# Kernel tuning notes

Measured on AMD Instinct MI355X. Metric: run time of the kernel, lower is better.

## Reference

```python
import jax, jax.numpy as jnp
import numpy as np

N, K = 8192, 32
DIM_INP_Q, DIM_INP_KV, DIM, DIM_OUT = 256, 256, 256, 512


def setup_inputs() -> dict:
    key = jax.random.key(0)
    ks = jax.random.split(key, 16)
    s = lambda k_, shp: jax.random.normal(k_, shp, dtype=jnp.float32) * 0.05
    return {
        "xyz_q": jax.random.normal(ks[0], (N, 3), dtype=jnp.float32),
        "feats_q": jax.random.normal(ks[1], (N, DIM_INP_Q), dtype=jnp.float32),
        "xyz_kv": jax.random.normal(ks[2], (N, K, 3), dtype=jnp.float32),
        "feats_kv": jax.random.normal(ks[3], (N, K, DIM_INP_KV), dtype=jnp.float32),
        # linear weights stored (in, out); y = x @ W + b
        "Wq": s(ks[4], (DIM_INP_Q, DIM)),
        "Wk": s(ks[5], (DIM_INP_KV, DIM)),
        "Wv": s(ks[6], (DIM_INP_KV, DIM)),
        "d1_w": s(ks[7], (3, DIM // 2)), "d1_b": jnp.zeros((DIM // 2,), jnp.float32),
        "d2_w": s(ks[8], (DIM // 2, DIM)), "d2_b": jnp.zeros((DIM,), jnp.float32),
        "g1_w": s(ks[9], (DIM, DIM)), "g1_b": jnp.zeros((DIM,), jnp.float32),
        "g2_w": s(ks[10], (DIM, DIM)), "g2_b": jnp.zeros((DIM,), jnp.float32),
        "out_w": s(ks[11], (DIM, DIM_OUT)), "out_b": jnp.zeros((DIM_OUT,), jnp.float32),
    }


def reference(xyz_q, feats_q, xyz_kv, feats_kv, Wq, Wk, Wv,
              d1_w, d1_b, d2_w, d2_b, g1_w, g1_b, g2_w, g2_b, out_w, out_b):
    q_attn = feats_q @ Wq                      # (N, dim)
    k_attn = feats_kv @ Wk                     # (N, k, dim)
    v_attn = feats_kv @ Wv                     # (N, k, dim)
    # relative-position MLP: (N, k, 3) -> (N, k, dim)
    rel = xyz_q[:, None, :] - xyz_kv
    pos_encode = jax.nn.relu(rel @ d1_w + d1_b) @ d2_w + d2_b
    # subtractive vector attention scores through fc_gamma MLP
    h = q_attn[:, None, :] - k_attn + pos_encode
    attn = jax.nn.relu(h @ g1_w + g1_b) @ g2_w + g2_b   # (N, k, dim)
    attn = jax.nn.softmax(attn, axis=-2)                # softmax over neighbors k
    res = jnp.einsum('nmf,nmf->nf', attn, v_attn + pos_encode)
    res = res @ out_w + out_b                           # (N, dim_out)
    return (xyz_q, res)
```

## Files before the change

kernel.cpp:

```cpp
#include <hip/hip_runtime.h>
#include <hip/hip_bf16.h>

#define NPTS 8192
#define KN   32
#define DIM  256
#define DH   128
#define DOUT 512

typedef __attribute__((ext_vector_type(8))) short bf16x8;
typedef __attribute__((ext_vector_type(4))) short short4v;
typedef __attribute__((ext_vector_type(4))) float f32x4;

#define MFMA16(a, b, c) __builtin_amdgcn_mfma_f32_16x16x32_bf16((a), (b), (c), 0, 0, 0)

__device__ __forceinline__ short f2b(float f) {
    __hip_bfloat16 h = __float2bfloat16(f);
    return *reinterpret_cast<short*>(&h);
}

#define WSO_QATTN 0u
#define WSO_RES   8388608u
#define WSO_WKT   16777216u
#define WSO_WVT   16908288u
#define WSO_G1T   17039360u
#define WSO_G2T   17170432u
#define WSO_D2T   17301504u
#define WSO_OWT   17367040u

extern "C" __global__ __launch_bounds__(256)
void prep_w(const float* __restrict__ Wk, const float* __restrict__ Wv,
            const float* __restrict__ g1w, const float* __restrict__ g2w,
            const float* __restrict__ d2w, const float* __restrict__ ow,
            short* __restrict__ wkT, short* __restrict__ wvT,
            short* __restrict__ g1T, short* __restrict__ g2T,
            short* __restrict__ d2T, short* __restrict__ owT)
{
    __shared__ float s_t[64][65];
    const int bid = blockIdx.x, t = threadIdx.x;
    const float* src; short* dst;
    int scols, dcols, O, I;
    bool neg = false;
    if (bid < 64) {
        const int mat = bid >> 4, tile = bid & 15;
        O = (tile >> 2) * 64; I = (tile & 3) * 64;
        scols = 256; dcols = 256;
        if (mat == 0)      { src = Wk;  dst = wkT; neg = true; }
        else if (mat == 1) { src = Wv;  dst = wvT; }
        else if (mat == 2) { src = g1w; dst = g1T; }
        else               { src = g2w; dst = g2T; }
    } else if (bid < 72) {
        const int tile = bid - 64;
        O = (tile >> 1) * 64; I = (tile & 1) * 64;
        src = d2w; dst = d2T; scols = 256; dcols = 128;
    } else {
        const int tile = bid - 72;
        O = (tile >> 2) * 64; I = (tile & 3) * 64;
        src = ow; dst = owT; scols = 512; dcols = 256;
    }
    #pragma unroll
    for (int rep = 0; rep < 16; ++rep) {
        const int lin = rep * 256 + t;
        s_t[lin >> 6][lin & 63] =
            src[(size_t)(I + (lin >> 6)) * scols + O + (lin & 63)];
    }
    __syncthreads();
    #pragma unroll
    for (int rep = 0; rep < 16; ++rep) {
        const int lin = rep * 256 + t;
        const int o = lin >> 6, i = lin & 63;
        float v = s_t[i][o];
        if (neg) v = -v;
        dst[(size_t)(O + o) * dcols + I + i] = f2b(v);
    }
}

extern "C" __global__ __launch_bounds__(256)
void prep_q(const float* __restrict__ feats_q, const float* __restrict__ Wq,
            const float* __restrict__ xyz_q, float* __restrict__ q_attn,
            float* __restrict__ out)
{
    const int b = blockIdx.x;
    const int t = threadIdx.x;
    if (b >= 256) {
        const int idx = (b - 256) * 256 + t;
        out[idx] = xyz_q[idx];
        return;
    }
    __shared__ float s_q[32][256];
    for (int j = 0; j < 32; ++j)
        s_q[j][t] = feats_q[(size_t)(b * 32 + j) * 256 + t];
    __syncthreads();
    float acc[32];
    #pragma unroll
    for (int pt = 0; pt < 32; ++pt) acc[pt] = 0.f;
    for (int k = 0; k < 256; k += 4) {
        float wv0 = Wq[(k + 0) * 256 + t];
        float wv1 = Wq[(k + 1) * 256 + t];
        float wv2 = Wq[(k + 2) * 256 + t];
        float wv3 = Wq[(k + 3) * 256 + t];
        #pragma unroll
        for (int pt = 0; pt < 32; ++pt) {
            const float4 sv = *(const float4*)&s_q[pt][k];
            acc[pt] = fmaf(sv.x, wv0, acc[pt]);
            acc[pt] = fmaf(sv.y, wv1, acc[pt]);
            acc[pt] = fmaf(sv.z, wv2, acc[pt]);
            acc[pt] = fmaf(sv.w, wv3, acc[pt]);
        }
    }
    #pragma unroll
    for (int pt = 0; pt < 32; ++pt)
        q_attn[(size_t)(b * 32 + pt) * 256 + t] = acc[pt];
}

extern "C" __global__ __launch_bounds__(512, 4)
void ctb_main(const float* __restrict__ xyz_q, const float* __restrict__ xyz_kv,
              const float* __restrict__ feats_kv,
              const float* __restrict__ d1w, const float* __restrict__ d1b,
              const float* __restrict__ d2b, const float* __restrict__ g1b,
              const float* __restrict__ g2b,
              const float* __restrict__ q_attn,
              const short* __restrict__ wkTn, const short* __restrict__ wvT,
              const short* __restrict__ g1T, const short* __restrict__ g2T,
              const short* __restrict__ d2T,
              float* __restrict__ res_ws)
{
    extern __shared__ short s_lds[];
    const int t    = threadIdx.x;
    const int w    = t >> 6;
    const int lane = t & 63;
    const int q    = lane >> 4;
    const int ln   = lane & 15;
    const int p0   = blockIdx.x * 2;
    const int colbase = 32 * w + ln;

    {
        const int srow = t >> 3;
        const int sc   = t & 7;
        const float* fp = feats_kv + ((size_t)p0 * KN + srow) * DIM + sc * 32;
        #pragma unroll
        for (int j = 0; j < 8; ++j) {
            const float4 v = *(const float4*)(fp + 4 * j);
            const int c = sc * 32 + 4 * j;
            short4v sv;
            sv[0] = f2b(v.x); sv[1] = f2b(v.y); sv[2] = f2b(v.z); sv[3] = f2b(v.w);
            *(short4v*)&s_lds[srow * 256 + (c ^ ((srow & 7) << 3))] = sv;
        }
        const int pt = srow >> 5;
        const float qx = xyz_q[(p0 + pt) * 3 + 0];
        const float qy = xyz_q[(p0 + pt) * 3 + 1];
        const float qz = xyz_q[(p0 + pt) * 3 + 2];
        const float* xk = xyz_kv + ((size_t)p0 * KN + srow) * 3;
        const float rx = qx - xk[0], ry = qy - xk[1], rz = qz - xk[2];
        #pragma unroll
        for (int j = 0; j < 16; ++j) {
            const int c = sc * 16 + j;
            const float v = fmaxf(fmaf(rx, d1w[c],
                                  fmaf(ry, d1w[DH + c],
                                  fmaf(rz, d1w[2 * DH + c], d1b[c]))), 0.f);
            s_lds[16384 + srow * 128 + (c ^ ((srow & 7) << 3))] = f2b(v);
        }
    }
    __syncthreads();

    f32x4 vp[4][2];
    #pragma unroll
    for (int nt = 0; nt < 2; ++nt) {
        const float bb = d2b[colbase + 16 * nt];
        #pragma unroll
        for (int mt = 0; mt < 4; ++mt) vp[mt][nt] = (f32x4){bb, bb, bb, bb};
    }
    #pragma unroll
    for (int ks = 0; ks < 4; ++ks) {
        bf16x8 ar[4];
        #pragma unroll
        for (int mt = 0; mt < 4; ++mt) {
            const int row = 16 * mt + ln;
            ar[mt] = *(const bf16x8*)&s_lds[16384 + row * 128 +
                                            ((32 * ks + 8 * q) ^ ((row & 7) << 3))];
        }
        #pragma unroll
        for (int nt = 0; nt < 2; ++nt) {
            const bf16x8 bb = *(const bf16x8*)(d2T + (colbase + 16 * nt) * DH +
                                               32 * ks + 8 * q);
            #pragma unroll
            for (int mt = 0; mt < 4; ++mt) vp[mt][nt] = MFMA16(ar[mt], bb, vp[mt][nt]);
        }
    }
    f32x4 hacc[4][2];
    {
        float qv[2][2];
        #pragma unroll
        for (int pt = 0; pt < 2; ++pt)
            #pragma unroll
            for (int nt = 0; nt < 2; ++nt)
                qv[pt][nt] = q_attn[(size_t)(p0 + pt) * DIM + colbase + 16 * nt];
        #pragma unroll
        for (int mt = 0; mt < 4; ++mt)
            #pragma unroll
            for (int nt = 0; nt < 2; ++nt)
                #pragma unroll
                for (int r = 0; r < 4; ++r)
                    hacc[mt][nt][r] = vp[mt][nt][r] + qv[mt >> 1][nt];
    }
    #pragma unroll
    for (int ks = 0; ks < 8; ++ks) {
        bf16x8 af[4];
        #pragma unroll
        for (int mt = 0; mt < 4; ++mt) {
            const int row = 16 * mt + ln;
            af[mt] = *(const bf16x8*)&s_lds[row * 256 +
                                            ((32 * ks + 8 * q) ^ ((row & 7) << 3))];
        }
        #pragma unroll
        for (int nt = 0; nt < 2; ++nt) {
            const int co = (colbase + 16 * nt) * DIM + 32 * ks + 8 * q;
            const bf16x8 bk = *(const bf16x8*)(wkTn + co);
            const bf16x8 bv = *(const bf16x8*)(wvT + co);
            #pragma unroll
            for (int mt = 0; mt < 4; ++mt) {
                hacc[mt][nt] = MFMA16(af[mt], bk, hacc[mt][nt]);
                vp[mt][nt]   = MFMA16(af[mt], bv, vp[mt][nt]);
            }
        }
    }
    __syncthreads();
    #pragma unroll
    for (int mt = 0; mt < 4; ++mt)
        #pragma unroll
        for (int nt = 0; nt < 2; ++nt)
            #pragma unroll
            for (int r = 0; r < 4; ++r) {
                const int row = 16 * mt + 4 * q + r;
                const int col = colbase + 16 * nt;
                s_lds[row * 256 + (col ^ ((row & 7) << 3))] = f2b(hacc[mt][nt][r]);
            }
    __syncthreads();

    {
        f32x4 tacc[4][2];
        #pragma unroll
        for (int nt = 0; nt < 2; ++nt) {
            const float bb = g1b[colbase + 16 * nt];
            #pragma unroll
            for (int mt = 0; mt < 4; ++mt) tacc[mt][nt] = (f32x4){bb, bb, bb, bb};
        }
        #pragma unroll
        for (int ks = 0; ks < 8; ++ks) {
            bf16x8 ah[4];
            #pragma unroll
            for (int mt = 0; mt < 4; ++mt) {
                const int row = 16 * mt + ln;
                ah[mt] = *(const bf16x8*)&s_lds[row * 256 +
                                                ((32 * ks + 8 * q) ^ ((row & 7) << 3))];
            }
            #pragma unroll
            for (int nt = 0; nt < 2; ++nt) {
                const bf16x8 bb = *(const bf16x8*)(g1T + (colbase + 16 * nt) * DIM +
                                                   32 * ks + 8 * q);
                #pragma unroll
                for (int mt = 0; mt < 4; ++mt)
                    tacc[mt][nt] = MFMA16(ah[mt], bb, tacc[mt][nt]);
            }
        }
        __syncthreads();
        #pragma unroll
        for (int mt = 0; mt < 4; ++mt)
            #pragma unroll
            for (int nt = 0; nt < 2; ++nt)
                #pragma unroll
                for (int r = 0; r < 4; ++r) {
                    const int row = 16 * mt + 4 * q + r;
                    const int col = colbase + 16 * nt;
                    s_lds[row * 256 + (col ^ ((row & 7) << 3))] =
                        f2b(fmaxf(tacc[mt][nt][r], 0.f));
                }
        __syncthreads();
    }

    {
        f32x4 ap[4][2];
        #pragma unroll
        for (int nt = 0; nt < 2; ++nt) {
            const float bb = g2b[colbase + 16 * nt];
            #pragma unroll
            for (int mt = 0; mt < 4; ++mt) ap[mt][nt] = (f32x4){bb, bb, bb, bb};
        }
        #pragma unroll
        for (int ks = 0; ks < 8; ++ks) {
            bf16x8 at[4];
            #pragma unroll
            for (int mt = 0; mt < 4; ++mt) {
                const int row = 16 * mt + ln;
                at[mt] = *(const bf16x8*)&s_lds[row * 256 +
                                                ((32 * ks + 8 * q) ^ ((row & 7) << 3))];
            }
            #pragma unroll
            for (int nt = 0; nt < 2; ++nt) {
                const bf16x8 bb = *(const bf16x8*)(g2T + (colbase + 16 * nt) * DIM +
                                                   32 * ks + 8 * q);
                #pragma unroll
                for (int mt = 0; mt < 4; ++mt)
                    ap[mt][nt] = MFMA16(at[mt], bb, ap[mt][nt]);
            }
        }

        #pragma unroll
        for (int pt = 0; pt < 2; ++pt)
            #pragma unroll
            for (int nt = 0; nt < 2; ++nt) {
                float m = -1e30f;
                #pragma unroll
                for (int m2 = 0; m2 < 2; ++m2)
                    #pragma unroll
                    for (int r = 0; r < 4; ++r)
                        m = fmaxf(m, ap[2 * pt + m2][nt][r]);
                m = fmaxf(m, __shfl_xor(m, 16, 64));
                m = fmaxf(m, __shfl_xor(m, 32, 64));
                float s = 0.f;
                #pragma unroll
                for (int m2 = 0; m2 < 2; ++m2)
                    #pragma unroll
                    for (int r = 0; r < 4; ++r) {
                        const float e = __expf(ap[2 * pt + m2][nt][r] - m);
                        ap[2 * pt + m2][nt][r] = e;
                        s += e;
                    }
                s += __shfl_xor(s, 16, 64);
                s += __shfl_xor(s, 32, 64);
                float racc = 0.f;
                #pragma unroll
                for (int m2 = 0; m2 < 2; ++m2)
                    #pragma unroll
                    for (int r = 0; r < 4; ++r)
                        racc = fmaf(ap[2 * pt + m2][nt][r], vp[2 * pt + m2][nt][r],
                                    racc);
                racc += __shfl_xor(racc, 16, 64);
                racc += __shfl_xor(racc, 32, 64);
                if (q == 0)
                    res_ws[(size_t)(p0 + pt) * DIM + colbase + 16 * nt] = racc / s;
            }
    }
}

extern "C" __global__ __launch_bounds__(256, 2)
void ctb_out(const float* __restrict__ res_ws, const short* __restrict__ owT,
             const float* __restrict__ ob, float* __restrict__ out)
{
    __shared__ __align__(16) short s_a[32][264];
    const int t = threadIdx.x, w = t >> 6, lane = t & 63, q = lane >> 4, ln = lane & 15;
    const int rowbase = blockIdx.x * 32;

    {
        const int row = t >> 3;
        const int c0  = (t & 7) * 32;
        const float* src = res_ws + (size_t)(rowbase + row) * DIM + c0;
        #pragma unroll
        for (int j = 0; j < 32; j += 4) {
            const float4 v = *(const float4*)(src + j);
            s_a[row][c0 + j + 0] = f2b(v.x);
            s_a[row][c0 + j + 1] = f2b(v.y);
            s_a[row][c0 + j + 2] = f2b(v.z);
            s_a[row][c0 + j + 3] = f2b(v.w);
        }
    }
    __syncthreads();

    bf16x8 af[2][8];
    #pragma unroll
    for (int mt = 0; mt < 2; ++mt)
        #pragma unroll
        for (int ks = 0; ks < 8; ++ks)
            af[mt][ks] = *(const bf16x8*)&s_a[16 * mt + ln][32 * ks + 8 * q];

    const int colbase = 128 * w + ln;
    f32x4 acc[2][8];
    #pragma unroll
    for (int nt = 0; nt < 8; ++nt) {
        const float bb = ob[colbase + 16 * nt];
        #pragma unroll
        for (int mt = 0; mt < 2; ++mt) acc[mt][nt] = (f32x4){bb, bb, bb, bb};
    }
    #pragma unroll
    for (int ks = 0; ks < 8; ++ks) {
        const short* bp = owT + 32 * ks + 8 * q;
        #pragma unroll
        for (int nt = 0; nt < 8; ++nt) {
            const bf16x8 bb = *(const bf16x8*)(bp + (colbase + 16 * nt) * DIM);
            #pragma unroll
            for (int mt = 0; mt < 2; ++mt)
                acc[mt][nt] = MFMA16(af[mt][ks], bb, acc[mt][nt]);
        }
    }
    float* o = out + (size_t)NPTS * 3;
    #pragma unroll
    for (int mt = 0; mt < 2; ++mt)
        #pragma unroll
        for (int nt = 0; nt < 8; ++nt)
            #pragma unroll
            for (int r = 0; r < 4; ++r) {
                const int row = 16 * mt + 4 * q + r;
                const int col = colbase + 16 * nt;
                o[(size_t)(rowbase + row) * DOUT + col] = acc[mt][nt][r];
            }
}

extern "C" void kernel_launch(void* const* d_in, const int* in_sizes, int n_in,
                              void* d_out, int out_size, void* d_ws, size_t ws_size,
                              hipStream_t stream) {
    const float* xyz_q    = (const float*)d_in[0];
    const float* feats_q  = (const float*)d_in[1];
    const float* xyz_kv   = (const float*)d_in[2];
    const float* feats_kv = (const float*)d_in[3];
    const float* Wq       = (const float*)d_in[4];
    const float* Wk       = (const float*)d_in[5];
    const float* Wv       = (const float*)d_in[6];
    const float* d1w      = (const float*)d_in[7];
    const float* d1b      = (const float*)d_in[8];
    const float* d2w      = (const float*)d_in[9];
    const float* d2b      = (const float*)d_in[10];
    const float* g1w      = (const float*)d_in[11];
    const float* g1b      = (const float*)d_in[12];
    const float* g2w      = (const float*)d_in[13];
    const float* g2b      = (const float*)d_in[14];
    const float* ow       = (const float*)d_in[15];
    const float* ob       = (const float*)d_in[16];
    float* out = (float*)d_out;

    char* ws = (char*)d_ws;
    float* q_attn = (float*)(ws + WSO_QATTN);
    float* res_ws = (float*)(ws + WSO_RES);
    short* wkT    = (short*)(ws + WSO_WKT);
    short* wvT    = (short*)(ws + WSO_WVT);
    short* g1T    = (short*)(ws + WSO_G1T);
    short* g2T    = (short*)(ws + WSO_G2T);
    short* d2T    = (short*)(ws + WSO_D2T);
    short* owT    = (short*)(ws + WSO_OWT);

    prep_w<<<dim3(104), dim3(256), 0, stream>>>(Wk, Wv, g1w, g2w, d2w, ow,
                                                wkT, wvT, g1T, g2T, d2T, owT);
    prep_q<<<dim3(352), dim3(256), 0, stream>>>(feats_q, Wq, xyz_q, q_attn, out);
    ctb_main<<<dim3(4096), dim3(512), 49152, stream>>>(
        xyz_q, xyz_kv, feats_kv, d1w, d1b, d2b, g1b, g2b,
        q_attn, wkT, wvT, g1T, g2T, d2T, res_ws);
    ctb_out<<<dim3(256), dim3(256), 0, stream>>>(res_ws, owT, ob, out);
}
```

Baseline: 785.6 us.

## Widen per-wave column tiles in main kernel and use MFMA for Q projection

The main kernel drops from 8 waves to 4 per block, and each wave now covers 64 output columns instead of 32, so every A-fragment LDS read feeds twice as many MFMAs. Launch bounds change to 256 threads with 2 blocks per CU, trading occupancy for more register reuse and higher register pressure. Separately, the Q projection is rewritten to use bf16 MFMA with a transposed bf16 copy of Wq made in the weight-prep kernel, replacing the scalar fp32 FMA loop at some cost in precision.

```diff
diff --git a/kernel.cpp b/kernel.cpp
--- a/kernel.cpp
+++ b/kernel.cpp
@@ -26,14 +26,17 @@
 #define WSO_G2T   17170432u
 #define WSO_D2T   17301504u
 #define WSO_OWT   17367040u
+#define WSO_WQT   17629184u
 
 extern "C" __global__ __launch_bounds__(256)
 void prep_w(const float* __restrict__ Wk, const float* __restrict__ Wv,
             const float* __restrict__ g1w, const float* __restrict__ g2w,
             const float* __restrict__ d2w, const float* __restrict__ ow,
+            const float* __restrict__ Wq,
             short* __restrict__ wkT, short* __restrict__ wvT,
             short* __restrict__ g1T, short* __restrict__ g2T,
-            short* __restrict__ d2T, short* __restrict__ owT)
+            short* __restrict__ d2T, short* __restrict__ owT,
+            short* __restrict__ wqT)
 {
     __shared__ float s_t[64][65];
     const int bid = blockIdx.x, t = threadIdx.x;
@@ -52,10 +55,14 @@
         const int tile = bid - 64;
         O = (tile >> 1) * 64; I = (tile & 1) * 64;
         src = d2w; dst = d2T; scols = 256; dcols = 128;
-    } else {
+    } else if (bid < 104) {
         const int tile = bid - 72;
         O = (tile >> 2) * 64; I = (tile & 3) * 64;
         src = ow; dst = owT; scols = 512; dcols = 256;
+    } else {
+        const int tile = bid - 104;
+        O = (tile >> 2) * 64; I = (tile & 3) * 64;
+        src = Wq; dst = wqT; scols = 256; dcols = 256;
     }
     #pragma unroll
     for (int rep = 0; rep < 16; ++rep) {
@@ -75,7 +82,7 @@
 }
 
 extern "C" __global__ __launch_bounds__(256)
-void prep_q(const float* __restrict__ feats_q, const float* __restrict__ Wq,
+void prep_q(const float* __restrict__ feats_q, const short* __restrict__ wqT,
             const float* __restrict__ xyz_q, float* __restrict__ q_attn,
             float* __restrict__ out)
 {
@@ -86,33 +93,61 @@
         out[idx] = xyz_q[idx];
         return;
     }
-    __shared__ float s_q[32][256];
-    for (int j = 0; j < 32; ++j)
-        s_q[j][t] = feats_q[(size_t)(b * 32 + j) * 256 + t];
-    __syncthreads();
-    float acc[32];
-    #pragma unroll
-    for (int pt = 0; pt < 32; ++pt) acc[pt] = 0.f;
-    for (int k = 0; k < 256; k += 4) {
-        float wv0 = Wq[(k + 0) * 256 + t];
-        float wv1 = Wq[(k + 1) * 256 + t];
-        float wv2 = Wq[(k + 2) * 256 + t];
-        float wv3 = Wq[(k + 3) * 256 + t];
-        #pragma unroll
-        for (int pt = 0; pt < 32; ++pt) {
-            const float4 sv = *(const float4*)&s_q[pt][k];
-            acc[pt] = fmaf(sv.x, wv0, acc[pt]);
-            acc[pt] = fmaf(sv.y, wv1, acc[pt]);
-            acc[pt] = fmaf(sv.z, wv2, acc[pt]);
-            acc[pt] = fmaf(sv.w, wv3, acc[pt]);
-        }
-    }
-    #pragma unroll
-    for (int pt = 0; pt < 32; ++pt)
-        q_attn[(size_t)(b * 32 + pt) * 256 + t] = acc[pt];
-}
-
-extern "C" __global__ __launch_bounds__(512, 4)
+    __shared__ __align__(16) short s_a[32][264];
+    const int w = t >> 6, lane = t & 63, q = lane >> 4, ln = lane & 15;
+    const int rowbase = b * 32;
+    {
+        const int row = t >> 3;
+        const int c0  = (t & 7) * 32;
+        const float* src = feats_q + (size_t)(rowbase + row) * DIM + c0;
+        #pragma unroll
+        for (int j = 0; j < 32; j += 4) {
+            const float4 v = *(const float4*)(src + j);
+            s_a[row][c0 + j + 0] = f2b(v.x);
+            s_a[row][c0 + j + 1] = f2b(v.y);
+            s_a[row][c0 + j + 2] = f2b(v.z);
+            s_a[row][c0 + j + 3] = f2b(v.w);
+        }
+    }
+    __syncthreads();
+
+    bf16x8 af[2][8];
+    #pragma unroll
+    for (int mt = 0; mt < 2; ++mt)
+        #pragma unroll
+        for (int ks = 0; ks < 8; ++ks)
+            af[mt][ks] = *(const bf16x8*)&s_a[16 * mt + ln][32 * ks + 8 * q];
+
+    const int colbase = 64 * w + ln;
+    f32x4 acc[2][4];
+    #pragma unroll
+    for (int nt = 0; nt < 4; ++nt)
+        #pragma unroll
+        for (int mt = 0; mt < 2; ++mt) acc[mt][nt] = (f32x4){0.f, 0.f, 0.f, 0.f};
+    #pragma unroll
+    for (int ks = 0; ks < 8; ++ks) {
+        const short* bp = wqT + 32 * ks + 8 * q;
+        #pragma unroll
+        for (int nt = 0; nt < 4; ++nt) {
+            const bf16x8 bb = *(const bf16x8*)(bp + (colbase + 16 * nt) * DIM);
+            #pragma unroll
+            for (int mt = 0; mt < 2; ++mt)
+                acc[mt][nt] = MFMA16(af[mt][ks], bb, acc[mt][nt]);
+        }
+    }
+    #pragma unroll
+    for (int mt = 0; mt < 2; ++mt)
+        #pragma unroll
+        for (int nt = 0; nt < 4; ++nt)
+            #pragma unroll
+            for (int r = 0; r < 4; ++r) {
+                const int row = 16 * mt + 4 * q + r;
+                q_attn[(size_t)(rowbase + row) * DIM + colbase + 16 * nt] =
+                    acc[mt][nt][r];
+            }
+}
+
+extern "C" __global__ __launch_bounds__(256, 2)
 void ctb_main(const float* __restrict__ xyz_q, const float* __restrict__ xyz_kv,
               const float* __restrict__ feats_kv,
               const float* __restrict__ d1w, const float* __restrict__ d1b,
@@ -131,16 +166,16 @@
     const int q    = lane >> 4;
     const int ln   = lane & 15;
     const int p0   = blockIdx.x * 2;
-    const int colbase = 32 * w + ln;
-
-    {
-        const int srow = t >> 3;
-        const int sc   = t & 7;
-        const float* fp = feats_kv + ((size_t)p0 * KN + srow) * DIM + sc * 32;
-        #pragma unroll
-        for (int j = 0; j < 8; ++j) {
-            const float4 v = *(const float4*)(fp + 4 * j);
-            const int c = sc * 32 + 4 * j;
+    const int colbase = 64 * w + ln;
+
+    {
+        const int srow = t >> 2;
+        const int sc   = t & 3;
+        const float* fp = feats_kv + ((size_t)p0 * KN + srow) * DIM;
+        #pragma unroll
+        for (int j = 0; j < 16; ++j) {
+            const int c = 4 * sc + 16 * j;
+            const float4 v = *(const float4*)(fp + c);
             short4v sv;
             sv[0] = f2b(v.x); sv[1] = f2b(v.y); sv[2] = f2b(v.z); sv[3] = f2b(v.w);
             *(short4v*)&s_lds[srow * 256 + (c ^ ((srow & 7) << 3))] = sv;
@@ -152,19 +187,24 @@
         const float* xk = xyz_kv + ((size_t)p0 * KN + srow) * 3;
         const float rx = qx - xk[0], ry = qy - xk[1], rz = qz - xk[2];
         #pragma unroll
-        for (int j = 0; j < 16; ++j) {
-            const int c = sc * 16 + j;
-            const float v = fmaxf(fmaf(rx, d1w[c],
-                                  fmaf(ry, d1w[DH + c],
-                                  fmaf(rz, d1w[2 * DH + c], d1b[c]))), 0.f);
-            s_lds[16384 + srow * 128 + (c ^ ((srow & 7) << 3))] = f2b(v);
-        }
-    }
-    __syncthreads();
-
-    f32x4 vp[4][2];
-    #pragma unroll
-    for (int nt = 0; nt < 2; ++nt) {
+        for (int j = 0; j < 8; ++j) {
+            const int c = 4 * sc + 16 * j;
+            short4v sv;
+            #pragma unroll
+            for (int e = 0; e < 4; ++e) {
+                const int cc = c + e;
+                sv[e] = f2b(fmaxf(fmaf(rx, d1w[cc],
+                                  fmaf(ry, d1w[DH + cc],
+                                  fmaf(rz, d1w[2 * DH + cc], d1b[cc]))), 0.f));
+            }
+            *(short4v*)&s_lds[16384 + srow * 128 + (c ^ ((srow & 7) << 3))] = sv;
+        }
+    }
+    __syncthreads();
+
+    f32x4 vp[4][4];
+    #pragma unroll
+    for (int nt = 0; nt < 4; ++nt) {
         const float bb = d2b[colbase + 16 * nt];
         #pragma unroll
         for (int mt = 0; mt < 4; ++mt) vp[mt][nt] = (f32x4){bb, bb, bb, bb};
@@ -179,25 +219,25 @@
                                             ((32 * ks + 8 * q) ^ ((row & 7) << 3))];
         }
         #pragma unroll
-        for (int nt = 0; nt < 2; ++nt) {
+        for (int nt = 0; nt < 4; ++nt) {
             const bf16x8 bb = *(const bf16x8*)(d2T + (colbase + 16 * nt) * DH +
                                                32 * ks + 8 * q);
             #pragma unroll
             for (int mt = 0; mt < 4; ++mt) vp[mt][nt] = MFMA16(ar[mt], bb, vp[mt][nt]);
         }
     }
-    f32x4 hacc[4][2];
-    {
-        float qv[2][2];
+    f32x4 hacc[4][4];
+    {
+        float qv[2][4];
         #pragma unroll
         for (int pt = 0; pt < 2; ++pt)
             #pragma unroll
-            for (int nt = 0; nt < 2; ++nt)
+            for (int nt = 0; nt < 4; ++nt)
                 qv[pt][nt] = q_attn[(size_t)(p0 + pt) * DIM + colbase + 16 * nt];
         #pragma unroll
         for (int mt = 0; mt < 4; ++mt)
             #pragma unroll
-            for (int nt = 0; nt < 2; ++nt)
+            for (int nt = 0; nt < 4; ++nt)
                 #pragma unroll
                 for (int r = 0; r < 4; ++r)
                     hacc[mt][nt][r] = vp[mt][nt][r] + qv[mt >> 1][nt];
@@ -212,7 +252,7 @@
                                             ((32 * ks + 8 * q) ^ ((row & 7) << 3))];
         }
         #pragma unroll
-        for (int nt = 0; nt < 2; ++nt) {
+        for (int nt = 0; nt < 4; ++nt) {
             const int co = (colbase + 16 * nt) * DIM + 32 * ks + 8 * q;
             const bf16x8 bk = *(const bf16x8*)(wkTn + co);
             const bf16x8 bv = *(const bf16x8*)(wvT + co);
@@ -227,7 +267,7 @@
     #pragma unroll
     for (int mt = 0; mt < 4; ++mt)
         #pragma unroll
-        for (int nt = 0; nt < 2; ++nt)
+        for (int nt = 0; nt < 4; ++nt)
             #pragma unroll
             for (int r = 0; r < 4; ++r) {
                 const int row = 16 * mt + 4 * q + r;
@@ -237,9 +277,9 @@
     __syncthreads();
 
     {
-        f32x4 tacc[4][2];
-        #pragma unroll
-        for (int nt = 0; nt < 2; ++nt) {
+        f32x4 tacc[4][4];
+        #pragma unroll
+        for (int nt = 0; nt < 4; ++nt) {
             const float bb = g1b[colbase + 16 * nt];
             #pragma unroll
             for (int mt = 0; mt < 4; ++mt) tacc[mt][nt] = (f32x4){bb, bb, bb, bb};
@@ -254,7 +294,7 @@
                                                 ((32 * ks + 8 * q) ^ ((row & 7) << 3))];
             }
             #pragma unroll
-            for (int nt = 0; nt < 2; ++nt) {
+            for (int nt = 0; nt < 4; ++nt) {
                 const bf16x8 bb = *(const bf16x8*)(g1T + (colbase + 16 * nt) * DIM +
                                                    32 * ks + 8 * q);
                 #pragma unroll
@@ -266,7 +306,7 @@
         #pragma unroll
         for (int mt = 0; mt < 4; ++mt)
             #pragma unroll
-            for (int nt = 0; nt < 2; ++nt)
+            for (int nt = 0; nt < 4; ++nt)
                 #pragma unroll
                 for (int r = 0; r < 4; ++r) {
                     const int row = 16 * mt + 4 * q + r;
@@ -278,9 +318,9 @@
     }
 
     {
-        f32x4 ap[4][2];
-        #pragma unroll
-        for (int nt = 0; nt < 2; ++nt) {
+        f32x4 ap[4][4];
+        #pragma unroll
+        for (int nt = 0; nt < 4; ++nt) {
             const float bb = g2b[colbase + 16 * nt];
             #pragma unroll
             for (int mt = 0; mt < 4; ++mt) ap[mt][nt] = (f32x4){bb, bb, bb, bb};
@@ -295,7 +335,7 @@
                                                 ((32 * ks + 8 * q) ^ ((row & 7) << 3))];
             }
             #pragma unroll
-            for (int nt = 0; nt < 2; ++nt) {
+            for (int nt = 0; nt < 4; ++nt) {
                 const bf16x8 bb = *(const bf16x8*)(g2T + (colbase + 16 * nt) * DIM +
                                                    32 * ks + 8 * q);
                 #pragma unroll
@@ -307,7 +347,7 @@
         #pragma unroll
         for (int pt = 0; pt < 2; ++pt)
             #pragma unroll
-            for (int nt = 0; nt < 2; ++nt) {
+            for (int nt = 0; nt < 4; ++nt) {
                 float m = -1e30f;
                 #pragma unroll
                 for (int m2 = 0; m2 < 2; ++m2)
@@ -435,11 +475,12 @@
     short* g2T    = (short*)(ws + WSO_G2T);
     short* d2T    = (short*)(ws + WSO_D2T);
     short* owT    = (short*)(ws + WSO_OWT);
-
-    prep_w<<<dim3(104), dim3(256), 0, stream>>>(Wk, Wv, g1w, g2w, d2w, ow,
-                                                wkT, wvT, g1T, g2T, d2T, owT);
-    prep_q<<<dim3(352), dim3(256), 0, stream>>>(feats_q, Wq, xyz_q, q_attn, out);
-    ctb_main<<<dim3(4096), dim3(512), 49152, stream>>>(
+    short* wqT    = (short*)(ws + WSO_WQT);
+
+    prep_w<<<dim3(120), dim3(256), 0, stream>>>(Wk, Wv, g1w, g2w, d2w, ow, Wq,
+                                                wkT, wvT, g1T, g2T, d2T, owT, wqT);
+    prep_q<<<dim3(352), dim3(256), 0, stream>>>(feats_q, wqT, xyz_q, q_attn, out);
+    ctb_main<<<dim3(4096), dim3(256), 49152, stream>>>(
         xyz_q, xyz_kv, feats_kv, d1w, d1b, d2b, g1b, g2b,
         q_attn, wkT, wvT, g1T, g2T, d2T, res_ws);
     ctb_out<<<dim3(256), dim3(256), 0, stream>>>(res_ws, owT, ob, out);
```

New measurement: 682.1 us. 1.15x faster.
